# Kernel optimization log

Hardware: AMD Instinct MI355X
Metric: run time of the kernel (lower is better)

The kernel has to match this reference:

```python
import jax, jax.numpy as jnp
import numpy as np

N = 100000      # nodes
E = 1600000     # edges
NFEAT = 200
NHID = 128
NOUT = 64
EPS = 1e-5      # BatchNorm eps


def setup_inputs() -> dict:
    key = jax.random.key(0)
    ks = jax.random.split(key, 12)

    def glorot(k, shape):
        fan_in, fan_out = shape
        lim = (6.0 / (fan_in + fan_out)) ** 0.5
        return jax.random.uniform(k, shape, jnp.float32, -lim, lim)

    return {
        "x": jax.random.normal(ks[0], (N, NFEAT), jnp.float32),
        "adj": jax.random.randint(ks[1], (2, E), 0, N, jnp.int64),
        "weight": jax.random.uniform(ks[2], (E,), jnp.float32),
        "W1": glorot(ks[3], (NFEAT, NHID)), "b1": jnp.zeros((NHID,), jnp.float32),
        "W2": glorot(ks[4], (NHID, NHID)), "b2": jnp.zeros((NHID,), jnp.float32),
        "g1": jnp.ones((NHID,), jnp.float32), "beta1": jnp.zeros((NHID,), jnp.float32),
        "g2": jnp.ones((NHID,), jnp.float32), "beta2": jnp.zeros((NHID,), jnp.float32),
        "fc1_W": glorot(ks[5], (NFEAT + 2 * NHID, NHID)), "fc1_b": jnp.zeros((NHID,), jnp.float32),
        "fc2_W": glorot(ks[6], (NHID, NOUT)), "fc2_b": jnp.zeros((NOUT,), jnp.float32),
    }


def gcn_conv(x, src, dst, ew, W, b):
    # PyG GCNConv: add self-loops (weight 1), symmetric normalization,
    # h = D^{-1/2} (A+I) D^{-1/2} (x W) + b. Aggregation at dst from src.
    h = x @ W                                   # [N, F_out]
    deg = jax.ops.segment_sum(ew, dst, num_segments=N)  # weighted in-degree (+1 self)
    dinv = jnp.where(deg > 0, jax.lax.rsqrt(deg), 0.0)
    norm = dinv[src] * ew * dinv[dst]           # [E+N]
    msg = h[src] * norm[:, None]                # [E+N, F_out] gather
    out = jax.ops.segment_sum(msg, dst, num_segments=N)  # scatter-add
    return out + b


def batch_norm(h, g, beta):
    m = h.mean(axis=0)
    v = jnp.mean(jnp.square(h - m), axis=0)
    return g * (h - m) * jax.lax.rsqrt(v + EPS) + beta


def reference(x, adj, weight, W1, b1, W2, b2, g1, beta1, g2, beta2,
              fc1_W, fc1_b, fc2_W, fc2_b):
    # add self-loops once (shared by both conv layers)
    loop = jnp.arange(N, dtype=adj.dtype)
    src = jnp.concatenate([adj[0], loop])
    dst = jnp.concatenate([adj[1], loop])
    ew = jnp.concatenate([weight, jnp.ones((N,), weight.dtype)])

    h1 = jax.nn.relu(gcn_conv(x, src, dst, ew, W1, b1))
    h1 = batch_norm(h1, g1, beta1)              # dropout = identity (eval)
    h2 = jax.nn.relu(gcn_conv(h1, src, dst, ew, W2, b2))
    h2 = batch_norm(h2, g2, beta2)

    cat = jnp.concatenate([x, h1, h2], axis=1)  # [N, nfeat + 2*nhid]
    out = jax.nn.relu(cat @ fc1_W + fc1_b)
    out = jax.nn.relu(out @ fc2_W + fc2_b)
    return out
```

## Files before the change

### kernel.cpp

```cpp
#include <hip/hip_runtime.h>
#include <hip/hip_bf16.h>

#define N_NODES 100000
#define N_EDGES 1600000
#define NFEAT   200
#define NHID    128
#define NOUT    64
#define BN_EPS  1e-5f

static constexpr int SCAN_NB = (N_NODES + 255) / 256;

__global__ __launch_bounds__(256) void init_kernel(int* counts, float* deg, float* stats)
{
    int i = blockIdx.x * 256 + threadIdx.x;
    if (i <= N_NODES) counts[i] = 0;
    if (i <  N_NODES) deg[i]    = 1.0f;
    if (i <  512)     stats[i]  = 0.0f;
}

__global__ __launch_bounds__(256) void hist_kernel(const int* __restrict__ adj,
                                                   const float* __restrict__ wt,
                                                   int* __restrict__ counts,
                                                   float* __restrict__ deg)
{
    int e = blockIdx.x * 256 + threadIdx.x;
    if (e >= N_EDGES) return;
    int d = adj[N_EDGES + e];
    atomicAdd(&counts[d], 1);
    atomicAdd(&deg[d], wt[e]);
}

__global__ __launch_bounds__(256) void dinv_kernel(float* deg)
{
    int i = blockIdx.x * 256 + threadIdx.x;
    if (i >= N_NODES) return;
    float d = deg[i];
    deg[i] = (d > 0.f) ? rsqrtf(d) : 0.f;
}

__global__ __launch_bounds__(256) void scan_block(const int* __restrict__ counts,
                                                  int* __restrict__ rowptr,
                                                  int* __restrict__ bsums)
{
    __shared__ int s[256];
    int t = threadIdx.x;
    int i = blockIdx.x * 256 + t;
    int v = (i < N_NODES) ? counts[i] : 0;
    s[t] = v; __syncthreads();
    #pragma unroll
    for (int off = 1; off < 256; off <<= 1) {
        int x = (t >= off) ? s[t - off] : 0;
        __syncthreads();
        s[t] += x;
        __syncthreads();
    }
    if (i < N_NODES) rowptr[i] = s[t] - v;
    if (t == 255) bsums[blockIdx.x] = s[255];
}

__global__ __launch_bounds__(512) void scan_top(int* bsums)
{
    __shared__ int s[512];
    int t = threadIdx.x;
    int v = (t < SCAN_NB) ? bsums[t] : 0;
    s[t] = v; __syncthreads();
    #pragma unroll
    for (int off = 1; off < 512; off <<= 1) {
        int x = (t >= off) ? s[t - off] : 0;
        __syncthreads();
        s[t] += x;
        __syncthreads();
    }
    if (t < SCAN_NB) bsums[t] = s[t] - v;
}

__global__ __launch_bounds__(256) void scan_add(int* __restrict__ rowptr,
                                                const int* __restrict__ bsums,
                                                int* __restrict__ cursor)
{
    int i = blockIdx.x * 256 + threadIdx.x;
    if (i < N_NODES) {
        int r = rowptr[i] + bsums[i >> 8];
        rowptr[i] = r;
        cursor[i] = r;
    }
    if (i == 0) rowptr[N_NODES] = N_EDGES;
}

__global__ __launch_bounds__(256) void fill_kernel(const int* __restrict__ adj,
                                                   const float* __restrict__ wt,
                                                   const float* __restrict__ dinv,
                                                   int* __restrict__ cursor,
                                                   int* __restrict__ col_src,
                                                   float* __restrict__ col_norm)
{
    int e = blockIdx.x * 256 + threadIdx.x;
    if (e >= N_EDGES) return;
    int s = adj[e];
    int d = adj[N_EDGES + e];
    int pos = atomicAdd(&cursor[d], 1);
    col_src[pos]  = s;
    col_norm[pos] = dinv[s] * wt[e] * dinv[d];
}

template<int NC, bool ACCUM, bool BIASRELU>
__global__ __launch_bounds__(256) void gemm_kernel(const float* __restrict__ A,
                                                   const float* __restrict__ W,
                                                   const float* __restrict__ bias,
                                                   float* __restrict__ C,
                                                   int M, int K)
{
    constexpr int BM = 64, BK = 64;
    constexpr int COLG = NC / 8;
    constexpr int RPT  = NC / 32;
    __shared__ float a_t[BM][BK + 1];
    __shared__ float w_t[BK][NC];

    int t  = threadIdx.x;
    int m0 = blockIdx.x * BM;
    int c0 = (t % COLG) * 8;
    int r0 = (t / COLG) * RPT;

    float acc[RPT][8];
    #pragma unroll
    for (int j = 0; j < RPT; ++j)
        #pragma unroll
        for (int i = 0; i < 8; ++i) acc[j][i] = 0.f;

    for (int k0 = 0; k0 < K; k0 += BK) {
        constexpr int WF4 = BK * NC / 4 / 256;
        #pragma unroll
        for (int i = 0; i < WF4; ++i) {
            int idx = t + i * 256;
            int kr  = idx / (NC / 4);
            int c4  = (idx % (NC / 4)) * 4;
            float4 v = make_float4(0.f, 0.f, 0.f, 0.f);
            if (k0 + kr < K) v = *(const float4*)&W[(size_t)(k0 + kr) * NC + c4];
            *(float4*)&w_t[kr][c4] = v;
        }
        #pragma unroll
        for (int i = 0; i < 4; ++i) {
            int idx = t + i * 256;
            int ar  = idx / 16;
            int ac  = (idx % 16) * 4;
            float4 v = make_float4(0.f, 0.f, 0.f, 0.f);
            int m = m0 + ar, k = k0 + ac;
            if (m < M && k < K) v = *(const float4*)&A[(size_t)m * K + k];
            a_t[ar][ac]     = v.x;
            a_t[ar][ac + 1] = v.y;
            a_t[ar][ac + 2] = v.z;
            a_t[ar][ac + 3] = v.w;
        }
        __syncthreads();

        #pragma unroll 8
        for (int kk = 0; kk < BK; ++kk) {
            float4 w0 = *(float4*)&w_t[kk][c0];
            float4 w1 = *(float4*)&w_t[kk][c0 + 4];
            #pragma unroll
            for (int j = 0; j < RPT; ++j) {
                float a = a_t[r0 + j][kk];
                acc[j][0] += a * w0.x; acc[j][1] += a * w0.y;
                acc[j][2] += a * w0.z; acc[j][3] += a * w0.w;
                acc[j][4] += a * w1.x; acc[j][5] += a * w1.y;
                acc[j][6] += a * w1.z; acc[j][7] += a * w1.w;
            }
        }
        __syncthreads();
    }

    float bi[8];
    if (BIASRELU) {
        #pragma unroll
        for (int i = 0; i < 8; ++i) bi[i] = bias[c0 + i];
    }
    #pragma unroll
    for (int j = 0; j < RPT; ++j) {
        int m = m0 + r0 + j;
        if (m >= M) continue;
        float o[8];
        #pragma unroll
        for (int i = 0; i < 8; ++i) o[i] = acc[j][i];
        if (ACCUM) {
            float4 p0 = *(float4*)&C[(size_t)m * NC + c0];
            float4 p1 = *(float4*)&C[(size_t)m * NC + c0 + 4];
            o[0] += p0.x; o[1] += p0.y; o[2] += p0.z; o[3] += p0.w;
            o[4] += p1.x; o[5] += p1.y; o[6] += p1.z; o[7] += p1.w;
        }
        if (BIASRELU) {
            #pragma unroll
            for (int i = 0; i < 8; ++i) o[i] = fmaxf(o[i] + bi[i], 0.f);
        }
        *(float4*)&C[(size_t)m * NC + c0]     = make_float4(o[0], o[1], o[2], o[3]);
        *(float4*)&C[(size_t)m * NC + c0 + 4] = make_float4(o[4], o[5], o[6], o[7]);
    }
}

__global__ __launch_bounds__(256) void agg_kernel(const float* __restrict__ h,
                                                  const float* __restrict__ bias,
                                                  const float* __restrict__ dinv,
                                                  const int* __restrict__ rowptr,
                                                  const int* __restrict__ col_src,
                                                  const float* __restrict__ col_norm,
                                                  float* __restrict__ out)
{
    int node = blockIdx.x * 4 + (threadIdx.x >> 6);
    if (node >= N_NODES) return;
    int lane = threadIdx.x & 63;
    int f0 = lane * 2;

    float di = dinv[node];
    float2 hv = *(const float2*)&h[(size_t)node * NHID + f0];
    float ax = di * di * hv.x;
    float ay = di * di * hv.y;

    int beg = rowptr[node], end = rowptr[node + 1];
    for (int e = beg; e < end; ++e) {
        int s = col_src[e];
        float nw = col_norm[e];
        float2 v = *(const float2*)&h[(size_t)s * NHID + f0];
        ax += nw * v.x;
        ay += nw * v.y;
    }
    float2 b = *(const float2*)&bias[f0];
    float2 o;
    o.x = fmaxf(ax + b.x, 0.f);
    o.y = fmaxf(ay + b.y, 0.f);
    *(float2*)&out[(size_t)node * NHID + f0] = o;
}

__global__ __launch_bounds__(256) void stats_kernel(const float* __restrict__ h,
                                                    float* __restrict__ st)
{
    __shared__ float ls[256], ls2[256];
    int t = threadIdx.x;
    int c = t & 127, half = t >> 7;
    float s = 0.f, s2 = 0.f;
    for (int r = blockIdx.x * 2 + half; r < N_NODES; r += gridDim.x * 2) {
        float v = h[(size_t)r * NHID + c];
        s += v; s2 += v * v;
    }
    ls[t] = s; ls2[t] = s2; __syncthreads();
    if (half == 0) {
        s  += ls[t + 128];
        s2 += ls2[t + 128];
        atomicAdd(&st[c], s);
        atomicAdd(&st[128 + c], s2);
    }
}

__global__ __launch_bounds__(128) void bn_finalize(const float* __restrict__ st,
                                                   const float* __restrict__ g,
                                                   const float* __restrict__ beta,
                                                   float* __restrict__ scsh)
{
    int c = threadIdx.x;
    float mean = st[c] / (float)N_NODES;
    float var  = st[128 + c] / (float)N_NODES - mean * mean;
    float inv  = rsqrtf(var + BN_EPS);
    float sc   = g[c] * inv;
    scsh[c]       = sc;
    scsh[128 + c] = beta[c] - mean * sc;
}

__global__ __launch_bounds__(256) void bn_apply(float* __restrict__ h,
                                                const float* __restrict__ scsh)
{
    size_t idx = (size_t)blockIdx.x * 256 + threadIdx.x;
    if (idx >= (size_t)N_NODES * (NHID / 4)) return;
    int c = (idx & (NHID / 4 - 1)) * 4;
    float4 sc = *(const float4*)&scsh[c];
    float4 sh = *(const float4*)&scsh[128 + c];
    float4 v  = *(float4*)&h[idx * 4];
    v.x = sc.x * v.x + sh.x;
    v.y = sc.y * v.y + sh.y;
    v.z = sc.z * v.z + sh.z;
    v.w = sc.w * v.w + sh.w;
    *(float4*)&h[idx * 4] = v;
}

extern "C" void kernel_launch(void* const* d_in, const int* in_sizes, int n_in,
                              void* d_out, int out_size, void* d_ws, size_t ws_size,
                              hipStream_t stream)
{
    const float* x     = (const float*)d_in[0];
    const int*   adj   = (const int*)d_in[1];
    const float* wt    = (const float*)d_in[2];
    const float* W1    = (const float*)d_in[3];
    const float* b1    = (const float*)d_in[4];
    const float* W2    = (const float*)d_in[5];
    const float* b2    = (const float*)d_in[6];
    const float* g1    = (const float*)d_in[7];
    const float* beta1 = (const float*)d_in[8];
    const float* g2    = (const float*)d_in[9];
    const float* beta2 = (const float*)d_in[10];
    const float* fc1W  = (const float*)d_in[11];
    const float* fc1b  = (const float*)d_in[12];
    const float* fc2W  = (const float*)d_in[13];
    const float* fc2b  = (const float*)d_in[14];
    float* out = (float*)d_out;

    char* p = (char*)d_ws;
    auto alloc = [&](size_t bytes) -> void* {
        void* r = (void*)p;
        p += (bytes + 255) & ~(size_t)255;
        return r;
    };
    float* dinv     = (float*)alloc((size_t)N_NODES * 4);
    int*   counts   = (int*)  alloc((size_t)(N_NODES + 1) * 4);
    int*   rowptr   = (int*)  alloc((size_t)(N_NODES + 1) * 4);
    int*   cursor   = (int*)  alloc((size_t)N_NODES * 4);
    int*   col_src  = (int*)  alloc((size_t)N_EDGES * 4);
    float* col_norm = (float*)alloc((size_t)N_EDGES * 4);
    int*   bsums    = (int*)  alloc(1024 * 4);
    float* stats    = (float*)alloc(512 * 4);
    float* scsh     = (float*)alloc(256 * 4);
    float* t_buf    = (float*)alloc((size_t)N_NODES * NHID * 4);
    float* h1       = (float*)alloc((size_t)N_NODES * NHID * 4);
    float* h2       = (float*)alloc((size_t)N_NODES * NHID * 4);

    const int gN  = (N_NODES + 255) / 256;
    const int gN1 = (N_NODES + 256) / 256;
    const int gE  = (N_EDGES + 255) / 256;
    const int gM  = (N_NODES + 63) / 64;

    init_kernel<<<gN1, 256, 0, stream>>>(counts, dinv, stats);
    hist_kernel<<<gE, 256, 0, stream>>>(adj, wt, counts, dinv);
    dinv_kernel<<<gN, 256, 0, stream>>>(dinv);
    scan_block<<<SCAN_NB, 256, 0, stream>>>(counts, rowptr, bsums);
    scan_top<<<1, 512, 0, stream>>>(bsums);
    scan_add<<<SCAN_NB, 256, 0, stream>>>(rowptr, bsums, cursor);
    fill_kernel<<<gE, 256, 0, stream>>>(adj, wt, dinv, cursor, col_src, col_norm);

    gemm_kernel<NHID, false, false><<<gM, 256, 0, stream>>>(x, W1, nullptr, t_buf, N_NODES, NFEAT);
    agg_kernel<<<(N_NODES + 3) / 4, 256, 0, stream>>>(t_buf, b1, dinv, rowptr, col_src, col_norm, h1);
    stats_kernel<<<1024, 256, 0, stream>>>(h1, stats);
    bn_finalize<<<1, 128, 0, stream>>>(stats, g1, beta1, scsh);
    bn_apply<<<(N_NODES * (NHID / 4) + 255) / 256, 256, 0, stream>>>(h1, scsh);

    gemm_kernel<NHID, false, false><<<gM, 256, 0, stream>>>(h1, W2, nullptr, t_buf, N_NODES, NHID);
    agg_kernel<<<(N_NODES + 3) / 4, 256, 0, stream>>>(t_buf, b2, dinv, rowptr, col_src, col_norm, h2);
    stats_kernel<<<1024, 256, 0, stream>>>(h2, stats + 256);
    bn_finalize<<<1, 128, 0, stream>>>(stats + 256, g2, beta2, scsh);
    bn_apply<<<(N_NODES * (NHID / 4) + 255) / 256, 256, 0, stream>>>(h2, scsh);

    gemm_kernel<NHID, false, false><<<gM, 256, 0, stream>>>(x,  fc1W,                    nullptr, t_buf, N_NODES, NFEAT);
    gemm_kernel<NHID, true,  false><<<gM, 256, 0, stream>>>(h1, fc1W + (size_t)NFEAT * NHID,          nullptr, t_buf, N_NODES, NHID);
    gemm_kernel<NHID, true,  true ><<<gM, 256, 0, stream>>>(h2, fc1W + (size_t)(NFEAT + NHID) * NHID, fc1b,    t_buf, N_NODES, NHID);

    gemm_kernel<NOUT, false, true><<<gM, 256, 0, stream>>>(t_buf, fc2W, fc2b, out, N_NODES, NHID);
}
```

Before: 1.299 ms.

## Fuse BatchNorm into GEMM loads, merge fc1 GEMMs, pack CSR edges

BatchNorm apply passes are removed and the scale/shift is applied while loading A tiles in the following GEMM, and inside a new fused fc1 kernel that reads x, h1 and h2 directly, replacing three accumulating GEMMs. CSR source and norm are packed into int2, aggregation is unrolled by four edges, and dinv is computed inside scan_add. The GEMM row tile grows to 128. This removes several full passes over the hidden-activation buffers, at the cost of redundant normalization work per GEMM tile and higher register use.

```diff
diff --git a/kernel.cpp b/kernel.cpp
--- a/kernel.cpp
+++ b/kernel.cpp
@@ -30,14 +30,6 @@
     atomicAdd(&deg[d], wt[e]);
 }
 
-__global__ __launch_bounds__(256) void dinv_kernel(float* deg)
-{
-    int i = blockIdx.x * 256 + threadIdx.x;
-    if (i >= N_NODES) return;
-    float d = deg[i];
-    deg[i] = (d > 0.f) ? rsqrtf(d) : 0.f;
-}
-
 __global__ __launch_bounds__(256) void scan_block(const int* __restrict__ counts,
                                                   int* __restrict__ rowptr,
                                                   int* __restrict__ bsums)
@@ -76,13 +68,16 @@
 
 __global__ __launch_bounds__(256) void scan_add(int* __restrict__ rowptr,
                                                 const int* __restrict__ bsums,
-                                                int* __restrict__ cursor)
+                                                int* __restrict__ cursor,
+                                                float* __restrict__ deg)
 {
     int i = blockIdx.x * 256 + threadIdx.x;
     if (i < N_NODES) {
         int r = rowptr[i] + bsums[i >> 8];
         rowptr[i] = r;
         cursor[i] = r;
+        float d = deg[i];
+        deg[i] = (d > 0.f) ? rsqrtf(d) : 0.f;
     }
     if (i == 0) rowptr[N_NODES] = N_EDGES;
 }
@@ -91,35 +86,39 @@
                                                    const float* __restrict__ wt,
                                                    const float* __restrict__ dinv,
                                                    int* __restrict__ cursor,
-                                                   int* __restrict__ col_src,
-                                                   float* __restrict__ col_norm)
+                                                   int2* __restrict__ col)
 {
     int e = blockIdx.x * 256 + threadIdx.x;
     if (e >= N_EDGES) return;
     int s = adj[e];
     int d = adj[N_EDGES + e];
     int pos = atomicAdd(&cursor[d], 1);
-    col_src[pos]  = s;
-    col_norm[pos] = dinv[s] * wt[e] * dinv[d];
-}
-
-template<int NC, bool ACCUM, bool BIASRELU>
+    int2 c;
+    c.x = s;
+    c.y = __float_as_int(dinv[s] * wt[e] * dinv[d]);
+    col[pos] = c;
+}
+
+template<int NC, bool BIASRELU, bool HASBN>
 __global__ __launch_bounds__(256) void gemm_kernel(const float* __restrict__ A,
                                                    const float* __restrict__ W,
                                                    const float* __restrict__ bias,
+                                                   const float* __restrict__ scsh,
                                                    float* __restrict__ C,
                                                    int M, int K)
 {
-    constexpr int BM = 64, BK = 64;
+    constexpr int BM = 128, BK = 64;
     constexpr int COLG = NC / 8;
-    constexpr int RPT  = NC / 32;
-    __shared__ float a_t[BM][BK + 1];
+    constexpr int RPT  = (BM * COLG) / 256;
+    __shared__ float a_t[BM][BK + 2];
     __shared__ float w_t[BK][NC];
 
-    int t  = threadIdx.x;
-    int m0 = blockIdx.x * BM;
-    int c0 = (t % COLG) * 8;
-    int r0 = (t / COLG) * RPT;
+    int t    = threadIdx.x;
+    int m0   = blockIdx.x * BM;
+    int g    = t % COLG;
+    int c_lo = g * 4;
+    int c_hi = NC / 2 + c_lo;
+    int r0   = (t / COLG) * RPT;
 
     float acc[RPT][8];
     #pragma unroll
@@ -139,13 +138,23 @@
             *(float4*)&w_t[kr][c4] = v;
         }
         #pragma unroll
-        for (int i = 0; i < 4; ++i) {
+        for (int i = 0; i < BM * BK / 4 / 256; ++i) {
             int idx = t + i * 256;
-            int ar  = idx / 16;
-            int ac  = (idx % 16) * 4;
+            int ar  = idx / (BK / 4);
+            int ac  = (idx % (BK / 4)) * 4;
             float4 v = make_float4(0.f, 0.f, 0.f, 0.f);
             int m = m0 + ar, k = k0 + ac;
-            if (m < M && k < K) v = *(const float4*)&A[(size_t)m * K + k];
+            if (m < M && k < K) {
+                v = *(const float4*)&A[(size_t)m * K + k];
+                if (HASBN) {
+                    float4 sc = *(const float4*)&scsh[k];
+                    float4 sh = *(const float4*)&scsh[NHID + k];
+                    v.x = v.x * sc.x + sh.x;
+                    v.y = v.y * sc.y + sh.y;
+                    v.z = v.z * sc.z + sh.z;
+                    v.w = v.w * sc.w + sh.w;
+                }
+            }
             a_t[ar][ac]     = v.x;
             a_t[ar][ac + 1] = v.y;
             a_t[ar][ac + 2] = v.z;
@@ -155,8 +164,8 @@
 
         #pragma unroll 8
         for (int kk = 0; kk < BK; ++kk) {
-            float4 w0 = *(float4*)&w_t[kk][c0];
-            float4 w1 = *(float4*)&w_t[kk][c0 + 4];
+            float4 w0 = *(float4*)&w_t[kk][c_lo];
+            float4 w1 = *(float4*)&w_t[kk][c_hi];
             #pragma unroll
             for (int j = 0; j < RPT; ++j) {
                 float a = a_t[r0 + j][kk];
@@ -169,30 +178,126 @@
         __syncthreads();
     }
 
-    float bi[8];
+    float4 b0, b1;
     if (BIASRELU) {
-        #pragma unroll
-        for (int i = 0; i < 8; ++i) bi[i] = bias[c0 + i];
+        b0 = *(const float4*)&bias[c_lo];
+        b1 = *(const float4*)&bias[c_hi];
     }
     #pragma unroll
     for (int j = 0; j < RPT; ++j) {
         int m = m0 + r0 + j;
         if (m >= M) continue;
-        float o[8];
-        #pragma unroll
-        for (int i = 0; i < 8; ++i) o[i] = acc[j][i];
-        if (ACCUM) {
-            float4 p0 = *(float4*)&C[(size_t)m * NC + c0];
-            float4 p1 = *(float4*)&C[(size_t)m * NC + c0 + 4];
-            o[0] += p0.x; o[1] += p0.y; o[2] += p0.z; o[3] += p0.w;
-            o[4] += p1.x; o[5] += p1.y; o[6] += p1.z; o[7] += p1.w;
-        }
+        float4 o0 = make_float4(acc[j][0], acc[j][1], acc[j][2], acc[j][3]);
+        float4 o1 = make_float4(acc[j][4], acc[j][5], acc[j][6], acc[j][7]);
         if (BIASRELU) {
+            o0.x = fmaxf(o0.x + b0.x, 0.f); o0.y = fmaxf(o0.y + b0.y, 0.f);
+            o0.z = fmaxf(o0.z + b0.z, 0.f); o0.w = fmaxf(o0.w + b0.w, 0.f);
+            o1.x = fmaxf(o1.x + b1.x, 0.f); o1.y = fmaxf(o1.y + b1.y, 0.f);
+            o1.z = fmaxf(o1.z + b1.z, 0.f); o1.w = fmaxf(o1.w + b1.w, 0.f);
+        }
+        *(float4*)&C[(size_t)m * NC + c_lo] = o0;
+        *(float4*)&C[(size_t)m * NC + c_hi] = o1;
+    }
+}
+
+__global__ __launch_bounds__(256) void fc1_kernel(const float* __restrict__ x,
+                                                  const float* __restrict__ h1,
+                                                  const float* __restrict__ s1,
+                                                  const float* __restrict__ h2,
+                                                  const float* __restrict__ s2,
+                                                  const float* __restrict__ W,
+                                                  const float* __restrict__ bias,
+                                                  float* __restrict__ C, int M)
+{
+    constexpr int NC = NHID, BM = 128, BK = 64, KTOT = NFEAT + 2 * NHID;
+    constexpr int COLG = NC / 8, RPT = (BM * COLG) / 256;
+    __shared__ float a_t[BM][BK + 2];
+    __shared__ float w_t[BK][NC];
+
+    int t    = threadIdx.x;
+    int m0   = blockIdx.x * BM;
+    int g    = t % COLG;
+    int c_lo = g * 4;
+    int c_hi = NC / 2 + c_lo;
+    int r0   = (t / COLG) * RPT;
+
+    float acc[RPT][8];
+    #pragma unroll
+    for (int j = 0; j < RPT; ++j)
+        #pragma unroll
+        for (int i = 0; i < 8; ++i) acc[j][i] = 0.f;
+
+    for (int k0 = 0; k0 < 512; k0 += BK) {
+        #pragma unroll
+        for (int i = 0; i < 8; ++i) {
+            int idx = t + i * 256;
+            int kr  = idx / (NC / 4);
+            int c4  = (idx % (NC / 4)) * 4;
+            float4 v = make_float4(0.f, 0.f, 0.f, 0.f);
+            if (k0 + kr < KTOT) v = *(const float4*)&W[(size_t)(k0 + kr) * NC + c4];
+            *(float4*)&w_t[kr][c4] = v;
+        }
+        #pragma unroll
+        for (int i = 0; i < BM * BK / 4 / 256; ++i) {
+            int idx = t + i * 256;
+            int ar  = idx / (BK / 4);
+            int ac  = (idx % (BK / 4)) * 4;
+            int m   = m0 + ar, kc = k0 + ac;
+            float4 v = make_float4(0.f, 0.f, 0.f, 0.f);
+            if (m < M) {
+                if (kc < NFEAT) {
+                    v = *(const float4*)&x[(size_t)m * NFEAT + kc];
+                } else if (kc < NFEAT + NHID) {
+                    int k = kc - NFEAT;
+                    v = *(const float4*)&h1[(size_t)m * NHID + k];
+                    float4 sc = *(const float4*)&s1[k];
+                    float4 sh = *(const float4*)&s1[NHID + k];
+                    v.x = v.x * sc.x + sh.x; v.y = v.y * sc.y + sh.y;
+                    v.z = v.z * sc.z + sh.z; v.w = v.w * sc.w + sh.w;
+                } else if (kc < KTOT) {
+                    int k = kc - NFEAT - NHID;
+                    v = *(const float4*)&h2[(size_t)m * NHID + k];
+                    float4 sc = *(const float4*)&s2[k];
+                    float4 sh = *(const float4*)&s2[NHID + k];
+                    v.x = v.x * sc.x + sh.x; v.y = v.y * sc.y + sh.y;
+                    v.z = v.z * sc.z + sh.z; v.w = v.w * sc.w + sh.w;
+                }
+            }
+            a_t[ar][ac]     = v.x;
+            a_t[ar][ac + 1] = v.y;
+            a_t[ar][ac + 2] = v.z;
+            a_t[ar][ac + 3] = v.w;
+        }
+        __syncthreads();
+
+        #pragma unroll 8
+        for (int kk = 0; kk < BK; ++kk) {
+            float4 w0 = *(float4*)&w_t[kk][c_lo];
+            float4 w1 = *(float4*)&w_t[kk][c_hi];
             #pragma unroll
-            for (int i = 0; i < 8; ++i) o[i] = fmaxf(o[i] + bi[i], 0.f);
-        }
-        *(float4*)&C[(size_t)m * NC + c0]     = make_float4(o[0], o[1], o[2], o[3]);
-        *(float4*)&C[(size_t)m * NC + c0 + 4] = make_float4(o[4], o[5], o[6], o[7]);
+            for (int j = 0; j < RPT; ++j) {
+                float a = a_t[r0 + j][kk];
+                acc[j][0] += a * w0.x; acc[j][1] += a * w0.y;
+                acc[j][2] += a * w0.z; acc[j][3] += a * w0.w;
+                acc[j][4] += a * w1.x; acc[j][5] += a * w1.y;
+                acc[j][6] += a * w1.z; acc[j][7] += a * w1.w;
+            }
+        }
+        __syncthreads();
+    }
+
+    float4 b0 = *(const float4*)&bias[c_lo];
+    float4 b1 = *(const float4*)&bias[c_hi];
+    #pragma unroll
+    for (int j = 0; j < RPT; ++j) {
+        int m = m0 + r0 + j;
+        if (m >= M) continue;
+        float4 o0 = make_float4(fmaxf(acc[j][0] + b0.x, 0.f), fmaxf(acc[j][1] + b0.y, 0.f),
+                                fmaxf(acc[j][2] + b0.z, 0.f), fmaxf(acc[j][3] + b0.w, 0.f));
+        float4 o1 = make_float4(fmaxf(acc[j][4] + b1.x, 0.f), fmaxf(acc[j][5] + b1.y, 0.f),
+                                fmaxf(acc[j][6] + b1.z, 0.f), fmaxf(acc[j][7] + b1.w, 0.f));
+        *(float4*)&C[(size_t)m * NC + c_lo] = o0;
+        *(float4*)&C[(size_t)m * NC + c_hi] = o1;
     }
 }
 
@@ -200,8 +305,7 @@
                                                   const float* __restrict__ bias,
                                                   const float* __restrict__ dinv,
                                                   const int* __restrict__ rowptr,
-                                                  const int* __restrict__ col_src,
-                                                  const float* __restrict__ col_norm,
+                                                  const int2* __restrict__ col,
                                                   float* __restrict__ out)
 {
     int node = blockIdx.x * 4 + (threadIdx.x >> 6);
@@ -214,13 +318,25 @@
     float ax = di * di * hv.x;
     float ay = di * di * hv.y;
 
-    int beg = rowptr[node], end = rowptr[node + 1];
-    for (int e = beg; e < end; ++e) {
-        int s = col_src[e];
-        float nw = col_norm[e];
-        float2 v = *(const float2*)&h[(size_t)s * NHID + f0];
-        ax += nw * v.x;
-        ay += nw * v.y;
+    int e = rowptr[node], end = rowptr[node + 1];
+    for (; e + 4 <= end; e += 4) {
+        int2 c0 = col[e],     c1 = col[e + 1];
+        int2 c2 = col[e + 2], c3 = col[e + 3];
+        float2 v0 = *(const float2*)&h[(size_t)c0.x * NHID + f0];
+        float2 v1 = *(const float2*)&h[(size_t)c1.x * NHID + f0];
+        float2 v2 = *(const float2*)&h[(size_t)c2.x * NHID + f0];
+        float2 v3 = *(const float2*)&h[(size_t)c3.x * NHID + f0];
+        float n0 = __int_as_float(c0.y), n1 = __int_as_float(c1.y);
+        float n2 = __int_as_float(c2.y), n3 = __int_as_float(c3.y);
+        ax += n0 * v0.x + n1 * v1.x + n2 * v2.x + n3 * v3.x;
+        ay += n0 * v0.y + n1 * v1.y + n2 * v2.y + n3 * v3.y;
+    }
+    for (; e < end; ++e) {
+        int2 c = col[e];
+        float2 v = *(const float2*)&h[(size_t)c.x * NHID + f0];
+        float n = __int_as_float(c.y);
+        ax += n * v.x;
+        ay += n * v.y;
     }
     float2 b = *(const float2*)&bias[f0];
     float2 o;
@@ -259,24 +375,8 @@
     float var  = st[128 + c] / (float)N_NODES - mean * mean;
     float inv  = rsqrtf(var + BN_EPS);
     float sc   = g[c] * inv;
-    scsh[c]       = sc;
-    scsh[128 + c] = beta[c] - mean * sc;
-}
-
-__global__ __launch_bounds__(256) void bn_apply(float* __restrict__ h,
-                                                const float* __restrict__ scsh)
-{
-    size_t idx = (size_t)blockIdx.x * 256 + threadIdx.x;
-    if (idx >= (size_t)N_NODES * (NHID / 4)) return;
-    int c = (idx & (NHID / 4 - 1)) * 4;
-    float4 sc = *(const float4*)&scsh[c];
-    float4 sh = *(const float4*)&scsh[128 + c];
-    float4 v  = *(float4*)&h[idx * 4];
-    v.x = sc.x * v.x + sh.x;
-    v.y = sc.y * v.y + sh.y;
-    v.z = sc.z * v.z + sh.z;
-    v.w = sc.w * v.w + sh.w;
-    *(float4*)&h[idx * 4] = v;
+    scsh[c]        = sc;
+    scsh[NHID + c] = beta[c] - mean * sc;
 }
 
 extern "C" void kernel_launch(void* const* d_in, const int* in_sizes, int n_in,
@@ -306,47 +406,41 @@
         p += (bytes + 255) & ~(size_t)255;
         return r;
     };
-    float* dinv     = (float*)alloc((size_t)N_NODES * 4);
-    int*   counts   = (int*)  alloc((size_t)(N_NODES + 1) * 4);
-    int*   rowptr   = (int*)  alloc((size_t)(N_NODES + 1) * 4);
-    int*   cursor   = (int*)  alloc((size_t)N_NODES * 4);
-    int*   col_src  = (int*)  alloc((size_t)N_EDGES * 4);
-    float* col_norm = (float*)alloc((size_t)N_EDGES * 4);
-    int*   bsums    = (int*)  alloc(1024 * 4);
-    float* stats    = (float*)alloc(512 * 4);
-    float* scsh     = (float*)alloc(256 * 4);
-    float* t_buf    = (float*)alloc((size_t)N_NODES * NHID * 4);
-    float* h1       = (float*)alloc((size_t)N_NODES * NHID * 4);
-    float* h2       = (float*)alloc((size_t)N_NODES * NHID * 4);
-
-    const int gN  = (N_NODES + 255) / 256;
+    float* dinv   = (float*)alloc((size_t)N_NODES * 4);
+    int*   counts = (int*)  alloc((size_t)(N_NODES + 1) * 4);
+    int*   rowptr = (int*)  alloc((size_t)(N_NODES + 1) * 4);
+    int*   cursor = (int*)  alloc((size_t)N_NODES * 4);
+    int2*  col    = (int2*) alloc((size_t)N_EDGES * 8);
+    int*   bsums  = (int*)  alloc(1024 * 4);
+    float* stats  = (float*)alloc(512 * 4);
+    float* scsh1  = (float*)alloc(256 * 4);
+    float* scsh2  = (float*)alloc(256 * 4);
+    float* t_buf  = (float*)alloc((size_t)N_NODES * NHID * 4);
+    float* h1     = (float*)alloc((size_t)N_NODES * NHID * 4);
+    float* h2     = (float*)alloc((size_t)N_NODES * NHID * 4);
+
     const int gN1 = (N_NODES + 256) / 256;
     const int gE  = (N_EDGES + 255) / 256;
-    const int gM  = (N_NODES + 63) / 64;
+    const int gM  = (N_NODES + 127) / 128;
 
     init_kernel<<<gN1, 256, 0, stream>>>(counts, dinv, stats);
     hist_kernel<<<gE, 256, 0, stream>>>(adj, wt, counts, dinv);
-    dinv_kernel<<<gN, 256, 0, stream>>>(dinv);
     scan_block<<<SCAN_NB, 256, 0, stream>>>(counts, rowptr, bsums);
     scan_top<<<1, 512, 0, stream>>>(bsums);
-    scan_add<<<SCAN_NB, 256, 0, stream>>>(rowptr, bsums, cursor);
-    fill_kernel<<<gE, 256, 0, stream>>>(adj, wt, dinv, cursor, col_src, col_norm);
-
-    gemm_kernel<NHID, false, false><<<gM, 256, 0, stream>>>(x, W1, nullptr, t_buf, N_NODES, NFEAT);
-    agg_kernel<<<(N_NODES + 3) / 4, 256, 0, stream>>>(t_buf, b1, dinv, rowptr, col_src, col_norm, h1);
+    scan_add<<<SCAN_NB, 256, 0, stream>>>(rowptr, bsums, cursor, dinv);
+    fill_kernel<<<gE, 256, 0, stream>>>(adj, wt, dinv, cursor, col);
+
+    gemm_kernel<NHID, false, false><<<gM, 256, 0, stream>>>(x, W1, nullptr, nullptr, t_buf, N_NODES, NFEAT);
+    agg_kernel<<<(N_NODES + 3) / 4, 256, 0, stream>>>(t_buf, b1, dinv, rowptr, col, h1);
     stats_kernel<<<1024, 256, 0, stream>>>(h1, stats);
-    bn_finalize<<<1, 128, 0, stream>>>(stats, g1, beta1, scsh);
-    bn_apply<<<(N_NODES * (NHID / 4) + 255) / 256, 256, 0, stream>>>(h1, scsh);
-
-    gemm_kernel<NHID, false, false><<<gM, 256, 0, stream>>>(h1, W2, nullptr, t_buf, N_NODES, NHID);
-    agg_kernel<<<(N_NODES + 3) / 4, 256, 0, stream>>>(t_buf, b2, dinv, rowptr, col_src, col_norm, h2);
+    bn_finalize<<<1, 128, 0, stream>>>(stats, g1, beta1, scsh1);
+
+    gemm_kernel<NHID, false, true><<<gM, 256, 0, stream>>>(h1, W2, nullptr, scsh1, t_buf, N_NODES, NHID);
+    agg_kernel<<<(N_NODES + 3) / 4, 256, 0, stream>>>(t_buf, b2, dinv, rowptr, col, h2);
     stats_kernel<<<1024, 256, 0, stream>>>(h2, stats + 256);
-    bn_finalize<<<1, 128, 0, stream>>>(stats + 256, g2, beta2, scsh);
-    bn_apply<<<(N_NODES * (NHID / 4) + 255) / 256, 256, 0, stream>>>(h2, scsh);
-
-    gemm_kernel<NHID, false, false><<<gM, 256, 0, stream>>>(x,  fc1W,                    nullptr, t_buf, N_NODES, NFEAT);
-    gemm_kernel<NHID, true,  false><<<gM, 256, 0, stream>>>(h1, fc1W + (size_t)NFEAT * NHID,          nullptr, t_buf, N_NODES, NHID);
-    gemm_kernel<NHID, true,  true ><<<gM, 256, 0, stream>>>(h2, fc1W + (size_t)(NFEAT + NHID) * NHID, fc1b,    t_buf, N_NODES, NHID);
-
-    gemm_kernel<NOUT, false, true><<<gM, 256, 0, stream>>>(t_buf, fc2W, fc2b, out, N_NODES, NHID);
-}
+    bn_finalize<<<1, 128, 0, stream>>>(stats + 256, g2, beta2, scsh2);
+
+    fc1_kernel<<<gM, 256, 0, stream>>>(x, h1, scsh1, h2, scsh2, fc1W, fc1b, t_buf, N_NODES);
+
+    gemm_kernel<NOUT, true, false><<<gM, 256, 0, stream>>>(t_buf, fc2W, fc2b, nullptr, out, N_NODES, NHID);
+}
```

After: 1.259 ms. -3.1%, faster.
